# Optimization experiments

Measured on AMD Instinct MI355X. Metric: run time of the kernel, lower is better.

Reference implementation:

```python
import jax, jax.numpy as jnp
import numpy as np

N = 50000
IN_C, HID_C, OUT_C = 512, 64, 40
E = 800000

def setup_inputs() -> dict:
    key = jax.random.key(0)
    ks = jax.random.split(key, 6)
    x = jax.random.normal(ks[0], (N, IN_C), dtype=jnp.float32)
    edge_index = jax.random.randint(ks[1], (2, E), 0, N, dtype=jnp.int64)
    # Glorot-style init for GCNConv linear weights, zero bias (PyG default)
    W1 = jax.random.normal(ks[2], (IN_C, HID_C), dtype=jnp.float32) / np.sqrt(IN_C)
    b1 = jnp.zeros((HID_C,), dtype=jnp.float32)
    W2 = jax.random.normal(ks[3], (HID_C, OUT_C), dtype=jnp.float32) / np.sqrt(HID_C)
    b2 = jnp.zeros((OUT_C,), dtype=jnp.float32)
    return {"x": x, "edge_index": edge_index, "W1": W1, "b1": b1, "W2": W2, "b2": b2}

def _gcn_conv(x, src, dst, W, b, n_nodes):
    # Standard GCNConv (self-loops already appended to src/dst):
    # h = x @ W; out[dst] += D^-1/2[src] * D^-1/2[dst] * h[src]; out += b
    h = x @ W
    deg = jnp.zeros((n_nodes,), dtype=h.dtype).at[dst].add(1.0)
    dinv = jnp.where(deg > 0, deg ** -0.5, 0.0)
    norm = dinv[src] * dinv[dst]                       # [E+N]
    msg = h[src] * norm[:, None]                       # gather + scale
    out = jax.ops.segment_sum(msg, dst, num_segments=n_nodes)
    return out + b

def reference(x, edge_index, W1, b1, W2, b2):
    n_nodes = x.shape[0]
    # add self-loops (PyG GCNConv default add_self_loops=True)
    loop = jnp.arange(n_nodes, dtype=edge_index.dtype)
    src = jnp.concatenate([edge_index[0], loop])
    dst = jnp.concatenate([edge_index[1], loop])
    # eval mode: dropout is identity
    h = _gcn_conv(x, src, dst, W1, b1, n_nodes)
    h = jax.nn.relu(h)
    h = _gcn_conv(h, src, dst, W2, b2, n_nodes)
    return jax.nn.softmax(h, axis=-1)
```

## Files before the change

### kernel.cpp

```cpp
#include <hip/hip_runtime.h>
#include <math.h>

#define IN_C 512
#define HID  64
#define OUTC 40

typedef __attribute__((ext_vector_type(8))) short bf16x8;
typedef __attribute__((ext_vector_type(4))) short bf16x4;
typedef __attribute__((ext_vector_type(4))) float f32x4;

#define GDEPTH 16

__device__ __forceinline__ ushort f2bf(float f) {
    uint u = __float_as_uint(f);
    u += 0x7FFFu + ((u >> 16) & 1u);
    return (ushort)(u >> 16);
}
__device__ __forceinline__ float bf2f(ushort s) {
    return __uint_as_float(((uint)s) << 16);
}

__global__ void k_zero(int4* __restrict__ p, int n4) {
    int i = blockIdx.x * blockDim.x + threadIdx.x;
    if (i < n4) p[i] = make_int4(0, 0, 0, 0);
}

__global__ void k_histsplit(const int* __restrict__ dst, int E,
                            int* __restrict__ cnt, int* __restrict__ rank,
                            int nbE2,
                            const float* __restrict__ W,
                            ushort* __restrict__ hi, ushort* __restrict__ lo) {
    if (blockIdx.x < (unsigned)nbE2) {
        int i = (blockIdx.x * blockDim.x + threadIdx.x) * 2;
        if (i < E) {
            if (i + 1 < E) {
                int2 d = *(const int2*)&dst[i];
                int r0 = atomicAdd(&cnt[d.x], 1);
                int r1 = atomicAdd(&cnt[d.y], 1);
                *(int2*)&rank[i] = make_int2(r0, r1);
            } else {
                rank[i] = atomicAdd(&cnt[dst[i]], 1);
            }
        }
    } else {
        int i = (blockIdx.x - nbE2) * blockDim.x + threadIdx.x;
        if (i >= HID * IN_C) return;
        int c = i >> 9, k = i & 511;
        float v = W[(size_t)k * HID + c];
        uint ub = __float_as_uint(v);
        uint hb = ub & 0xFFFF0000u;
        float lf = v - __uint_as_float(hb);
        int pidx = (k >> 5) * 2048 + c * 32 + (k & 31);
        hi[pidx] = (ushort)(ub >> 16);
        lo[pidx] = (ushort)(__float_as_uint(lf) >> 16);
    }
}

__global__ void k_scan1(const int* __restrict__ cnt, int N,
                        int* __restrict__ rowptr, int* __restrict__ bsum) {
    __shared__ int s[256];
    int t = threadIdx.x;
    int i = blockIdx.x * 256 + t;
    int v = (i < N) ? cnt[i] : 0;
    int x = v;
    s[t] = x; __syncthreads();
    #pragma unroll
    for (int o = 1; o < 256; o <<= 1) {
        int y = (t >= o) ? s[t - o] : 0;
        __syncthreads();
        x += y; s[t] = x;
        __syncthreads();
    }
    if (i < N) rowptr[i] = x - v;
    if (t == 255) bsum[blockIdx.x] = x;
}

__global__ void k_scan23(int* __restrict__ rowptr, const int* __restrict__ bsum,
                         const int* __restrict__ cnt, float* __restrict__ dinv,
                         int N, int E, int nb) {
    __shared__ int s[256];
    int t = threadIdx.x;
    int v = (t < nb) ? bsum[t] : 0;
    int x = v;
    s[t] = x; __syncthreads();
    #pragma unroll
    for (int o = 1; o < 256; o <<= 1) {
        int y = (t >= o) ? s[t - o] : 0;
        __syncthreads();
        x += y; s[t] = x;
        __syncthreads();
    }
    int bpre = (blockIdx.x > 0) ? s[blockIdx.x - 1] : 0;
    int i = blockIdx.x * 256 + t;
    if (i < N) {
        rowptr[i] += bpre;
        dinv[i] = rsqrtf(1.0f + (float)cnt[i]);
        if (i == 0) rowptr[N] = E;
    }
}

__global__ __launch_bounds__(256) void k_gemm1fill(
        const float* __restrict__ x,
        const ushort* __restrict__ Bphi, const ushort* __restrict__ Bplo,
        const float* __restrict__ dinv, ushort* __restrict__ h1s,
        int N, int nbG,
        const int* __restrict__ src, const int* __restrict__ dst,
        const int* __restrict__ rank, int E,
        const int* __restrict__ rowptr, int* __restrict__ ssort) {
    __shared__ ushort Ah[2][64 * 40], Al[2][64 * 40];
    __shared__ ushort Bh[2][64 * 40], Bl[2][64 * 40];

    if (blockIdx.x >= (unsigned)nbG) {
        int i = ((blockIdx.x - nbG) * blockDim.x + threadIdx.x) * 2;
        if (i >= E) return;
        if (i + 1 < E) {
            int2 d = *(const int2*)&dst[i];
            int2 s = *(const int2*)&src[i];
            int2 r = *(const int2*)&rank[i];
            ssort[rowptr[d.x] + r.x] = s.x;
            ssort[rowptr[d.y] + r.y] = s.y;
        } else {
            ssort[rowptr[dst[i]] + rank[i]] = src[i];
        }
        return;
    }

    int t = threadIdx.x;
    int wid = t >> 6, lane = t & 63;
    int lr = lane & 15, lko = lane >> 4;
    int wm = wid >> 1, wn = wid & 1;
    int row0 = blockIdx.x * 64;

    int srow = t >> 3, sf4 = t & 7;
    int scol = t >> 2, sseg = t & 3;
    int xr0 = row0 + srow;      if (xr0 >= N) xr0 = N - 1;
    int xr1 = row0 + srow + 32; if (xr1 >= N) xr1 = N - 1;
    const float* xp0 = x + (size_t)xr0 * IN_C + sf4 * 4;
    const float* xp1 = x + (size_t)xr1 * IN_C + sf4 * 4;
    const ushort* bhp = Bphi + scol * 32 + sseg * 8;
    const ushort* blp = Bplo + scol * 32 + sseg * 8;

    f32x4 acc[2][2] = {};
    float4 xrg[2];
    bf16x8 bhr, blr;

    auto stage_load = [&](int tile) {
        xrg[0] = *(const float4*)(xp0 + tile * 32);
        xrg[1] = *(const float4*)(xp1 + tile * 32);
        bhr = *(const bf16x8*)(bhp + tile * 2048);
        blr = *(const bf16x8*)(blp + tile * 2048);
    };
    auto stage_write = [&](int b) {
        #pragma unroll
        for (int p = 0; p < 2; ++p) {
            float xv[4];
            *(float4*)xv = xrg[p];
            bf16x4 h, l;
            #pragma unroll
            for (int j = 0; j < 4; ++j) {
                uint ub = __float_as_uint(xv[j]);
                float hf = __uint_as_float(ub & 0xFFFF0000u);
                float lf = xv[j] - hf;
                h[j] = (short)(ub >> 16);
                l[j] = (short)(__float_as_uint(lf) >> 16);
            }
            int row = srow + p * 32;
            *(bf16x4*)&Ah[b][row * 40 + sf4 * 4] = h;
            *(bf16x4*)&Al[b][row * 40 + sf4 * 4] = l;
        }
        *(bf16x8*)&Bh[b][scol * 40 + sseg * 8] = bhr;
        *(bf16x8*)&Bl[b][scol * 40 + sseg * 8] = blr;
    };
    auto compute = [&](int b) {
        bf16x8 afh[2], afl[2], bfh[2], bfl[2];
        #pragma unroll
        for (int mf = 0; mf < 2; ++mf) {
            int row = wm * 32 + mf * 16 + lr;
            afh[mf] = *(const bf16x8*)&Ah[b][row * 40 + lko * 8];
            afl[mf] = *(const bf16x8*)&Al[b][row * 40 + lko * 8];
        }
        #pragma unroll
        for (int nf = 0; nf < 2; ++nf) {
            int col = wn * 32 + nf * 16 + lr;
            bfh[nf] = *(const bf16x8*)&Bh[b][col * 40 + lko * 8];
            bfl[nf] = *(const bf16x8*)&Bl[b][col * 40 + lko * 8];
        }
        #pragma unroll
        for (int mf = 0; mf < 2; ++mf)
            #pragma unroll
            for (int nf = 0; nf < 2; ++nf) {
                acc[mf][nf] = __builtin_amdgcn_mfma_f32_16x16x32_bf16(afh[mf], bfh[nf], acc[mf][nf], 0, 0, 0);
                acc[mf][nf] = __builtin_amdgcn_mfma_f32_16x16x32_bf16(afl[mf], bfh[nf], acc[mf][nf], 0, 0, 0);
                acc[mf][nf] = __builtin_amdgcn_mfma_f32_16x16x32_bf16(afh[mf], bfl[nf], acc[mf][nf], 0, 0, 0);
            }
    };

    stage_load(0);
    stage_write(0);
    __syncthreads();

    #pragma unroll
    for (int i = 0; i < 16; ++i) {
        if (i < 15) stage_load(i + 1);
        compute(i & 1);
        if (i < 15) stage_write((i + 1) & 1);
        __syncthreads();
    }

    #pragma unroll
    for (int mf = 0; mf < 2; ++mf)
        #pragma unroll
        for (int r = 0; r < 4; ++r) {
            int orow = row0 + wm * 32 + mf * 16 + lko * 4 + r;
            if (orow < N) {
                float dv = dinv[orow];
                #pragma unroll
                for (int nf = 0; nf < 2; ++nf)
                    h1s[(size_t)orow * HID + wn * 32 + nf * 16 + lr] = f2bf(dv * acc[mf][nf][r]);
            }
        }
}

__global__ __launch_bounds__(256) void k_agg1g2(const ushort* __restrict__ h1s,
                                                const int* __restrict__ rowptr,
                                                const int* __restrict__ ssort,
                                                const float* __restrict__ dinv,
                                                const float* __restrict__ b1,
                                                const float* __restrict__ W2,
                                                ushort* __restrict__ h2s, int N) {
    __shared__ float wl[HID * OUTC];
    int t = threadIdx.x;
    #pragma unroll
    for (int q0 = 0; q0 < 3; ++q0) {
        int q = t + q0 * 256;
        if (q < 640) *(float4*)&wl[q * 4] = *(const float4*)&W2[q * 4];
    }
    __syncthreads();

    int lane = t & 63;
    int wq = t >> 6;
    int lc = lane < OUTC ? lane : 0;
    float bias = b1[lane];
    int nq = (N + 3) >> 2;

    for (int q = blockIdx.x; q < nq; q += gridDim.x) {
        int node = q * 4 + wq;
        if (node >= N) continue;
        float s0 = bf2f(h1s[(size_t)node * HID + lane]);
        float sv[GDEPTH];
        #pragma unroll
        for (int k = 0; k < GDEPTH; ++k) sv[k] = 0.f;
        int eu = __builtin_amdgcn_readfirstlane(rowptr[node]);
        int endu = __builtin_amdgcn_readfirstlane(rowptr[node + 1]);
        for (int e = eu; e < endu; e += GDEPTH) {
            int raw[GDEPTH];
            #pragma unroll
            for (int k = 0; k < GDEPTH; ++k) raw[k] = ssort[e + k];
            #pragma unroll
            for (int k = 0; k < GDEPTH; ++k) {
                int ix = (e + k < endu) ? raw[k] : raw[0];
                float v = bf2f(h1s[(size_t)ix * HID + lane]);
                sv[k] += (e + k < endu) ? v : 0.f;
            }
        }
        float s = s0;
        #pragma unroll
        for (int k = 0; k < GDEPTH; ++k) s += sv[k];
        float dv = dinv[node];
        float a = fmaxf(fmaf(dv, s, bias), 0.0f);
        float acc = 0.f;
        #pragma unroll
        for (int k = 0; k < HID; ++k) {
            float ak = __uint_as_float(__builtin_amdgcn_readlane(__float_as_uint(a), k));
            acc = fmaf(ak, wl[k * OUTC + lc], acc);
        }
        if (lane < OUTC) h2s[(size_t)node * OUTC + lane] = f2bf(dv * acc);
    }
}

__global__ __launch_bounds__(256) void k_agg2(const ushort* __restrict__ h2s,
                                              const int* __restrict__ rowptr,
                                              const int* __restrict__ ssort,
                                              const float* __restrict__ dinv,
                                              const float* __restrict__ b2,
                                              float* __restrict__ out, int N) {
    int lane = threadIdx.x & 63;
    int node = blockIdx.x * 4 + (threadIdx.x >> 6);
    if (node >= N) return;
    bool act = lane < OUTC;
    int lc = act ? lane : 0;
    float s0 = bf2f(h2s[(size_t)node * OUTC + lc]);
    float sv[GDEPTH];
    #pragma unroll
    for (int k = 0; k < GDEPTH; ++k) sv[k] = 0.f;
    int eu = __builtin_amdgcn_readfirstlane(rowptr[node]);
    int endu = __builtin_amdgcn_readfirstlane(rowptr[node + 1]);
    for (int e = eu; e < endu; e += GDEPTH) {
        int raw[GDEPTH];
        #pragma unroll
        for (int k = 0; k < GDEPTH; ++k) raw[k] = ssort[e + k];
        #pragma unroll
        for (int k = 0; k < GDEPTH; ++k) {
            int ix = (e + k < endu) ? raw[k] : raw[0];
            float v = bf2f(h2s[(size_t)ix * OUTC + lc]);
            sv[k] += (e + k < endu) ? v : 0.f;
        }
    }
    float s = s0;
    #pragma unroll
    for (int k = 0; k < GDEPTH; ++k) s += sv[k];
    float v = act ? (dinv[node] * s + b2[lane]) : -INFINITY;
    float m = v;
    #pragma unroll
    for (int o = 32; o; o >>= 1) m = fmaxf(m, __shfl_xor(m, o));
    float p = act ? expf(v - m) : 0.0f;
    float su = p;
    #pragma unroll
    for (int o = 32; o; o >>= 1) su += __shfl_xor(su, o);
    if (act) out[(size_t)node * OUTC + lane] = p / su;
}

static inline size_t alignup(size_t v) { return (v + 255) & ~(size_t)255; }

extern "C" void kernel_launch(void* const* d_in, const int* in_sizes, int n_in,
                              void* d_out, int out_size, void* d_ws, size_t ws_size,
                              hipStream_t stream) {
    const float* x  = (const float*)d_in[0];
    const int*   ei = (const int*)d_in[1];
    const float* W1 = (const float*)d_in[2];
    const float* b1 = (const float*)d_in[3];
    const float* W2 = (const float*)d_in[4];
    const float* b2 = (const float*)d_in[5];

    const int N = in_sizes[0] / IN_C;
    const int E = in_sizes[1] / 2;
    const int* src = ei;
    const int* dst = ei + E;

    char* w = (char*)d_ws;
    int* cnt    = (int*)w;   w += alignup((size_t)N * 4);
    int* rank   = (int*)w;   w += alignup((size_t)E * 4 + 256);
    int* rowptr = (int*)w;   w += alignup((size_t)(N + 1) * 4);
    int* bsum   = (int*)w;   w += alignup(256 * 4);
    int* ssort  = (int*)w;   w += alignup((size_t)E * 4 + 256);
    float* dinv = (float*)w; w += alignup((size_t)N * 4);
    ushort* h1s = (ushort*)w; w += alignup((size_t)N * HID * 2);
    ushort* h2s = (ushort*)w; w += alignup((size_t)N * OUTC * 2);
    ushort* Bphi = (ushort*)w; w += alignup((size_t)HID * IN_C * 2);
    ushort* Bplo = (ushort*)w; w += alignup((size_t)HID * IN_C * 2);

    const int n4 = (N + 3) / 4;
    k_zero<<<(n4 + 255) / 256, 256, 0, stream>>>((int4*)cnt, n4);

    const int nb   = (N + 255) / 256;
    const int nbE2 = (E / 2 + 255) / 256;
    const int nbW  = (HID * IN_C + 255) / 256;
    k_histsplit<<<nbE2 + nbW, 256, 0, stream>>>(dst, E, cnt, rank, nbE2, W1, Bphi, Bplo);
    k_scan1 <<<nb, 256, 0, stream>>>(cnt, N, rowptr, bsum);
    k_scan23<<<nb, 256, 0, stream>>>(rowptr, bsum, cnt, dinv, N, E, nb);

    const int nbG = (N + 63) / 64;
    k_gemm1fill<<<nbG + nbE2, 256, 0, stream>>>(x, Bphi, Bplo, dinv, h1s, N, nbG,
                                                src, dst, rank, E, rowptr, ssort);
    k_agg1g2<<<2048, 256, 0, stream>>>(h1s, rowptr, ssort, dinv, b1, W2, h2s, N);
    k_agg2  <<<(N + 3) / 4, 256, 0, stream>>>(h2s, rowptr, ssort, dinv, b2, (float*)d_out, N);
}
```

Before: 143.9 us.

## Stage GEMM1 tiles via direct global-to-LDS loads with XOR-swizzled layouts

```diff
diff --git a/kernel.cpp b/kernel.cpp
--- a/kernel.cpp
+++ b/kernel.cpp
@@ -6,7 +6,6 @@
 #define OUTC 40
 
 typedef __attribute__((ext_vector_type(8))) short bf16x8;
-typedef __attribute__((ext_vector_type(4))) short bf16x4;
 typedef __attribute__((ext_vector_type(4))) float f32x4;
 
 #define GDEPTH 16
@@ -18,6 +17,13 @@
 }
 __device__ __forceinline__ float bf2f(ushort s) {
     return __uint_as_float(((uint)s) << 16);
+}
+
+__device__ __forceinline__ void gl_lds16(const void* g, void* l) {
+    __builtin_amdgcn_global_load_lds(
+        (const __attribute__((address_space(1))) void*)g,
+        (__attribute__((address_space(3))) void*)l,
+        16, 0, 0);
 }
 
 __global__ void k_zero(int4* __restrict__ p, int n4) {
@@ -50,7 +56,9 @@
         uint ub = __float_as_uint(v);
         uint hb = ub & 0xFFFF0000u;
         float lf = v - __uint_as_float(hb);
-        int pidx = (k >> 5) * 2048 + c * 32 + (k & 31);
+        int lb = c * 64 + (k & 31) * 2;
+        int pb = lb ^ (((lb >> 6) & 7) << 4);
+        int pidx = (k >> 5) * 2048 + (pb >> 1);
         hi[pidx] = (ushort)(ub >> 16);
         lo[pidx] = (ushort)(__float_as_uint(lf) >> 16);
     }
@@ -107,8 +115,8 @@
         const int* __restrict__ src, const int* __restrict__ dst,
         const int* __restrict__ rank, int E,
         const int* __restrict__ rowptr, int* __restrict__ ssort) {
-    __shared__ ushort Ah[2][64 * 40], Al[2][64 * 40];
-    __shared__ ushort Bh[2][64 * 40], Bl[2][64 * 40];
+    __shared__ float  Af[2][2048];
+    __shared__ ushort Bh[2][2048], Bl[2][2048];
 
     if (blockIdx.x >= (unsigned)nbG) {
         int i = ((blockIdx.x - nbG) * blockDim.x + threadIdx.x) * 2;
@@ -131,59 +139,53 @@
     int wm = wid >> 1, wn = wid & 1;
     int row0 = blockIdx.x * 64;
 
-    int srow = t >> 3, sf4 = t & 7;
-    int scol = t >> 2, sseg = t & 3;
-    int xr0 = row0 + srow;      if (xr0 >= N) xr0 = N - 1;
-    int xr1 = row0 + srow + 32; if (xr1 >= N) xr1 = N - 1;
-    const float* xp0 = x + (size_t)xr0 * IN_C + sf4 * 4;
-    const float* xp1 = x + (size_t)xr1 * IN_C + sf4 * 4;
-    const ushort* bhp = Bphi + scol * 32 + sseg * 8;
-    const ushort* blp = Bplo + scol * 32 + sseg * 8;
+    int p0 = (wid * 64 + lane) * 16;
+    int r0l = p0 >> 7;
+    int o0 = p0 ^ ((r0l & 7) << 4);
+    int g0 = row0 + r0l; if (g0 >= N) g0 = N - 1;
+    const char* xsrc0 = (const char*)x + (size_t)g0 * 2048 + (o0 & 127);
+    int p1 = p0 + 4096;
+    int r1l = p1 >> 7;
+    int o1 = p1 ^ ((r1l & 7) << 4);
+    int g1 = row0 + r1l; if (g1 >= N) g1 = N - 1;
+    const char* xsrc1 = (const char*)x + (size_t)g1 * 2048 + (o1 & 127);
+    const char* bsrcH = (const char*)Bphi + (size_t)(wid * 64 + lane) * 16;
+    const char* bsrcL = (const char*)Bplo + (size_t)(wid * 64 + lane) * 16;
 
     f32x4 acc[2][2] = {};
-    float4 xrg[2];
-    bf16x8 bhr, blr;
-
-    auto stage_load = [&](int tile) {
-        xrg[0] = *(const float4*)(xp0 + tile * 32);
-        xrg[1] = *(const float4*)(xp1 + tile * 32);
-        bhr = *(const bf16x8*)(bhp + tile * 2048);
-        blr = *(const bf16x8*)(blp + tile * 2048);
-    };
-    auto stage_write = [&](int b) {
-        #pragma unroll
-        for (int p = 0; p < 2; ++p) {
-            float xv[4];
-            *(float4*)xv = xrg[p];
-            bf16x4 h, l;
-            #pragma unroll
-            for (int j = 0; j < 4; ++j) {
-                uint ub = __float_as_uint(xv[j]);
-                float hf = __uint_as_float(ub & 0xFFFF0000u);
-                float lf = xv[j] - hf;
-                h[j] = (short)(ub >> 16);
-                l[j] = (short)(__float_as_uint(lf) >> 16);
-            }
-            int row = srow + p * 32;
-            *(bf16x4*)&Ah[b][row * 40 + sf4 * 4] = h;
-            *(bf16x4*)&Al[b][row * 40 + sf4 * 4] = l;
-        }
-        *(bf16x8*)&Bh[b][scol * 40 + sseg * 8] = bhr;
-        *(bf16x8*)&Bl[b][scol * 40 + sseg * 8] = blr;
+
+    auto stage = [&](int tile, int b) {
+        gl_lds16(xsrc0 + (size_t)tile * 128, (char*)&Af[b][0] + wid * 1024);
+        gl_lds16(xsrc1 + (size_t)tile * 128, (char*)&Af[b][0] + 4096 + wid * 1024);
+        gl_lds16(bsrcH + (size_t)tile * 4096, (char*)&Bh[b][0] + wid * 1024);
+        gl_lds16(bsrcL + (size_t)tile * 4096, (char*)&Bl[b][0] + wid * 1024);
     };
     auto compute = [&](int b) {
         bf16x8 afh[2], afl[2], bfh[2], bfl[2];
         #pragma unroll
         for (int mf = 0; mf < 2; ++mf) {
             int row = wm * 32 + mf * 16 + lr;
-            afh[mf] = *(const bf16x8*)&Ah[b][row * 40 + lko * 8];
-            afl[mf] = *(const bf16x8*)&Al[b][row * 40 + lko * 8];
+            int fi = (row * 32 + lko * 8) ^ ((row & 7) << 2);
+            f32x4 a0 = *(const f32x4*)&Af[b][fi];
+            f32x4 a1 = *(const f32x4*)&Af[b][fi ^ 4];
+            float av[8];
+            *(f32x4*)&av[0] = a0;
+            *(f32x4*)&av[4] = a1;
+            #pragma unroll
+            for (int j = 0; j < 8; ++j) {
+                uint ub = __float_as_uint(av[j]);
+                float hf = __uint_as_float(ub & 0xFFFF0000u);
+                float lf = av[j] - hf;
+                afh[mf][j] = (short)(ub >> 16);
+                afl[mf][j] = (short)(__float_as_uint(lf) >> 16);
+            }
         }
         #pragma unroll
         for (int nf = 0; nf < 2; ++nf) {
             int col = wn * 32 + nf * 16 + lr;
-            bfh[nf] = *(const bf16x8*)&Bh[b][col * 40 + lko * 8];
-            bfl[nf] = *(const bf16x8*)&Bl[b][col * 40 + lko * 8];
+            int ci = (col * 32 + lko * 8) ^ ((col & 7) << 3);
+            bfh[nf] = *(const bf16x8*)&Bh[b][ci];
+            bfl[nf] = *(const bf16x8*)&Bl[b][ci];
         }
         #pragma unroll
         for (int mf = 0; mf < 2; ++mf)
@@ -195,15 +197,13 @@
             }
     };
 
-    stage_load(0);
-    stage_write(0);
+    stage(0, 0);
     __syncthreads();
 
     #pragma unroll
     for (int i = 0; i < 16; ++i) {
-        if (i < 15) stage_load(i + 1);
+        if (i < 15) stage(i + 1, (i + 1) & 1);
         compute(i & 1);
-        if (i < 15) stage_write((i + 1) & 1);
         __syncthreads();
     }
 
```

New measurement: 143.0 us. About the same (-0.6%).
